# Kernel optimization log

Hardware: AMD Instinct MI355X
Metric: run time of the kernel (lower is better)

The kernel has to match this reference:

```python
import jax, jax.numpy as jnp
import numpy as np

B, N, K, E, H, A = 16384, 200000, 16, 256, 2, 64
HD = E // H  # head_dim = 128


def setup_inputs() -> dict:
    key = jax.random.key(0)
    ks = jax.random.split(key, 10)
    s = 0.02
    return {
        "center_idx": jax.random.randint(ks[0], (B,), 0, N),
        "emb_table": jax.random.normal(ks[1], (N, E), jnp.float32),
        "neighbor_idx": jax.random.randint(ks[2], (N, K), 0, N),
        "neighbor_wt": jax.random.uniform(ks[3], (N, K), dtype=jnp.float32),
        # per-head attention MLP: Linear(2E -> A), GELU, Linear(A -> 1); stacked over heads
        "attn_W1": jax.random.normal(ks[4], (H, 2 * E, A), jnp.float32) * s,
        "attn_b1": jnp.zeros((H, A), jnp.float32),
        "attn_W2": jax.random.normal(ks[5], (H, A), jnp.float32) * s,
        "attn_b2": jnp.zeros((H,), jnp.float32),
        # per-head gate: Linear(HD -> HD), torch convention y = x @ W.T + b
        "gate_W": jax.random.normal(ks[6], (H, HD, HD), jnp.float32) * s,
        "gate_b": jnp.zeros((H, HD), jnp.float32),
        "out_W": jax.random.normal(ks[7], (E, E), jnp.float32) * s,
        "out_b": jnp.zeros((E,), jnp.float32),
    }


def reference(center_idx, emb_table, neighbor_idx, neighbor_wt,
              attn_W1, attn_b1, attn_W2, attn_b2,
              gate_W, gate_b, out_W, out_b):
    valid = center_idx >= 0                                      # [B]
    safe = jnp.maximum(center_idx, 0)
    center = jnp.where(valid[:, None], emb_table[safe], 0.0)      # [B,E]

    nb_idx = neighbor_idx[safe]                                   # [B,K]
    nb_wt = neighbor_wt[safe]                                     # [B,K]
    nb_mask = nb_idx >= 0
    nb_emb = emb_table[jnp.maximum(nb_idx, 0)]                    # [B,K,E]

    pair = jnp.concatenate(
        [jnp.broadcast_to(center[:, None, :], nb_emb.shape), nb_emb], axis=-1)  # [B,K,2E]

    # both attention heads in one einsum (exact GELU, as torch nn.GELU default)
    h1 = jax.nn.gelu(jnp.einsum('bkf,hfa->bkha', pair, attn_W1) + attn_b1,
                     approximate=False)                           # [B,K,H,A]
    logits = jnp.einsum('bkha,ha->bhk', h1, attn_W2) + attn_b2[None, :, None]  # [B,H,K]
    logits = logits + jnp.log(nb_wt + 1e-8)[:, None, :]
    logits = jnp.where(nb_mask[:, None, :], logits, -jnp.inf)
    has_any = jnp.any(nb_mask, axis=-1)                           # [B]
    logits = jnpp_where = jnp.where(has_any[:, None, None], logits, 0.0)
    w = jax.nn.softmax(logits, axis=-1)                           # [B,H,K]; dropout is identity in eval

    # aggregated[:, h*HD:(h+1)*HD] for head h == head-block of head-h weighted sum
    nb_r = nb_emb.reshape(-1, K, H, HD)
    agg = jnp.einsum('bhk,bkhd->bhd', w, nb_r)                    # [B,H,HD]

    c_head = center.reshape(-1, H, HD)
    gate = jax.nn.sigmoid(jnp.einsum('bhd,hed->bhe', c_head, gate_W) + gate_b)
    combined = (c_head + gate * agg).reshape(-1, E)               # [B,E]

    out = combined @ out_W.T + out_b
    return jnp.where(valid[:, None], out, center)
```

## Files before the change

### kernel.cpp

```cpp
#include <hip/hip_runtime.h>
#include <hip/hip_bf16.h>
#include <math.h>

#define BATCH   16384
#define NTAB    200000
#define KNB     16
#define EDIM    256
#define HEADS   2
#define ADIM    64
#define HD      128

typedef __attribute__((ext_vector_type(8))) short  short8;
typedef __attribute__((ext_vector_type(4))) float  f32x4;
typedef __attribute__((ext_vector_type(8))) unsigned short ushort8;
typedef __attribute__((ext_vector_type(4))) unsigned short ushort4v;

__device__ __forceinline__ unsigned short f2b(float f) {
    union { float f; unsigned u; } x; x.f = f;
    unsigned r = x.u + 0x7fffu + ((x.u >> 16) & 1u);
    return (unsigned short)(r >> 16);
}
__device__ __forceinline__ float b2f(unsigned short h) {
    union { unsigned u; float f; } x; x.u = ((unsigned)h) << 16;
    return x.f;
}

static const size_t OFF_T    = 0;
static const size_t OFF_CG   = OFF_T    + (size_t)NTAB * 128 * 2;
static const size_t OFF_COMB = OFF_CG   + (size_t)BATCH * 384 * 2;
static const size_t OFF_WCAT = OFF_COMB + (size_t)BATCH * 256 * 2;
static const size_t OFF_W1B  = OFF_WCAT + 384 * 256 * 2;
static const size_t OFF_OUTW = OFF_W1B  + 128 * 256 * 2;
static const size_t OFF_BCAT = OFF_OUTW + 256 * 256 * 2;

__global__ __launch_bounds__(256) void repack_kernel(
    const float* __restrict__ W1, const float* __restrict__ gateW,
    const float* __restrict__ outW,
    const float* __restrict__ b1, const float* __restrict__ gateB,
    unsigned short* __restrict__ WcatT, unsigned short* __restrict__ W1bT,
    unsigned short* __restrict__ outWT, float* __restrict__ bcat)
{
    int i = blockIdx.x * 256 + threadIdx.x;
    {
        int c = i >> 8, f = i & 255;
        float v;
        if (c < 128) {
            int h = c >> 6, a = c & 63;
            v = W1[h * 32768 + f * 64 + a];
        } else {
            int e = c - 128;
            int h = e >> 7;
            v = ((e >> 7) == (f >> 7)) ? gateW[h * 16384 + (e & 127) * 128 + (f & 127)] : 0.f;
        }
        WcatT[i] = f2b(v);
    }
    if (i < 32768) {
        int c = i >> 8, f = i & 255;
        int h = c >> 6, a = c & 63;
        W1bT[i] = f2b(W1[h * 32768 + (256 + f) * 64 + a]);
    }
    if (i < 65536) outWT[i] = f2b(outW[i]);
    if (i < 384) bcat[i] = (i < 128) ? b1[i] : gateB[i - 128];
}

template<int AMODE, bool OUT_BF16, bool HAS_BIAS, bool HAS_MASK>
__global__ __launch_bounds__(256) void gemm_mfma(
    const float* __restrict__ Af, const unsigned short* __restrict__ Ab,
    const int* __restrict__ gather,
    const unsigned short* __restrict__ Wt, int Nw,
    const float* __restrict__ bias, const int* __restrict__ mask,
    void* __restrict__ Cout, int M)
{
    __shared__ unsigned short sA[128 * 40];
    __shared__ unsigned short sB[128 * 32];
    __shared__ int s_idx[128];

    const int t = threadIdx.x;
    const int row0    = blockIdx.x * 128;
    const int colBase = blockIdx.y * 128;

    if (AMODE == 1 && t < 128) s_idx[t] = gather[row0 + t];

    const int wv   = t >> 6;
    const int wr   = wv >> 1, wc = wv & 1;
    const int lane = t & 63;
    const int l15  = lane & 15;
    const int quad = lane >> 4;

    f32x4 acc[4][4];
#pragma unroll
    for (int a = 0; a < 4; ++a)
#pragma unroll
        for (int b = 0; b < 4; ++b) acc[a][b] = (f32x4)0.f;

    for (int k0 = 0; k0 < 256; k0 += 32) {
        __syncthreads();
        if (AMODE == 2) {
#pragma unroll
            for (int l = 0; l < 2; ++l) {
                int p = t + l * 256;
                int row = p >> 2, seg = p & 3;
                int sr = row0 + row; if (sr > M - 1) sr = M - 1;
                ushort8 v = *(const ushort8*)&Ab[(size_t)sr * 256 + k0 + seg * 8];
                *(ushort8*)&sA[row * 40 + seg * 8] = v;
            }
        } else {
#pragma unroll
            for (int l = 0; l < 4; ++l) {
                int p = t + l * 256;
                int row = p >> 3, seg = p & 7;
                int sr;
                if (AMODE == 1) { int g = s_idx[row]; sr = g < 0 ? 0 : g; }
                else            { sr = row0 + row; if (sr > M - 1) sr = M - 1; }
                const float4 v = *(const float4*)&Af[(size_t)sr * 256 + k0 + seg * 4];
                ushort4v h;
                h.x = f2b(v.x); h.y = f2b(v.y); h.z = f2b(v.z); h.w = f2b(v.w);
                *(ushort4v*)&sA[row * 40 + seg * 4] = h;
            }
        }
#pragma unroll
        for (int l = 0; l < 2; ++l) {
            int p = t + l * 256;
            int n = p >> 2, seg = p & 3;
            const unsigned short* gsrc = Wt + (size_t)(colBase + n) * 256 + k0 + seg * 8;
            unsigned short* lbase = sB + (size_t)(p & ~63) * 8;
            __builtin_amdgcn_global_load_lds(
                (const __attribute__((address_space(1))) void*)gsrc,
                (__attribute__((address_space(3))) void*)lbase, 16, 0, 0);
        }
        __syncthreads();

        short8 af[4], bfr[4];
#pragma unroll
        for (int tr = 0; tr < 4; ++tr)
            af[tr] = *(const short8*)&sA[(wr * 64 + tr * 16 + l15) * 40 + quad * 8];
#pragma unroll
        for (int tc = 0; tc < 4; ++tc)
            bfr[tc] = *(const short8*)&sB[(wc * 64 + tc * 16 + l15) * 32 + quad * 8];
#pragma unroll
        for (int tr = 0; tr < 4; ++tr)
#pragma unroll
            for (int tc = 0; tc < 4; ++tc)
                acc[tr][tc] = __builtin_amdgcn_mfma_f32_16x16x32_bf16(
                    af[tr], bfr[tc], acc[tr][tc], 0, 0, 0);
    }

    float bcol[4];
#pragma unroll
    for (int tc = 0; tc < 4; ++tc)
        bcol[tc] = HAS_BIAS ? bias[colBase + wc * 64 + tc * 16 + l15] : 0.f;

#pragma unroll
    for (int tr = 0; tr < 4; ++tr) {
#pragma unroll
        for (int r = 0; r < 4; ++r) {
            int rowg = row0 + wr * 64 + tr * 16 + quad * 4 + r;
            if (rowg < M) {
                bool zero = HAS_MASK && (mask[rowg] < 0);
#pragma unroll
                for (int tc = 0; tc < 4; ++tc) {
                    int col = colBase + wc * 64 + tc * 16 + l15;
                    float v = zero ? 0.f : acc[tr][tc][r] + bcol[tc];
                    if (OUT_BF16)
                        ((unsigned short*)Cout)[(size_t)rowg * Nw + col] = f2b(v);
                    else
                        ((float*)Cout)[(size_t)rowg * Nw + col] = v;
                }
            }
        }
    }
}

__global__ __launch_bounds__(256) void epilogue_kernel(
    const float* __restrict__ table, const int* __restrict__ center_idx,
    const int* __restrict__ nb_idx_tab, const float* __restrict__ nb_wt_tab,
    const unsigned short* __restrict__ T, const unsigned short* __restrict__ cg,
    const float* __restrict__ W2, const float* __restrict__ b2,
    unsigned short* __restrict__ comb)
{
    const int b = blockIdx.x;
    const int t = threadIdx.x;

    __shared__ float s_cg[384];
    __shared__ float s_w2[128];
    __shared__ float s_logit[32];
    __shared__ float s_wmx[32];
    __shared__ int   s_nb[16];
    __shared__ float s_wt[16];

    const int ci   = center_idx[b];
    const int safe = ci < 0 ? 0 : ci;

    if (t < 16) {
        s_nb[t] = nb_idx_tab[(size_t)safe * KNB + t];
        s_wt[t] = nb_wt_tab[(size_t)safe * KNB + t];
    }
    if (t < 128) s_w2[t] = W2[t];
    for (int i = t; i < 384; i += 256) s_cg[i] = b2f(cg[(size_t)b * 384 + i]);
    const float ctr = (ci < 0) ? 0.f : table[(size_t)ci * 256 + t];
    __syncthreads();

    {
        const int k = t >> 4, s = t & 15;
        const int nb = s_nb[k];
        const int ns = nb < 0 ? 0 : nb;
        const ushort8 tv = *(const ushort8*)&T[(size_t)ns * 128 + s * 8];
        float partial = 0.f;
#pragma unroll
        for (int j = 0; j < 8; ++j) {
            int c = s * 8 + j;
            float v = b2f(tv[j]) + s_cg[c];
            float g = 0.5f * v * (1.f + erff(v * 0.70710678118654752440f));
            partial = fmaf(g, s_w2[c], partial);
        }
        partial += __shfl_xor(partial, 1, 64);
        partial += __shfl_xor(partial, 2, 64);
        partial += __shfl_xor(partial, 4, 64);
        if (s == 0) s_logit[k] = partial;
        if (s == 8) s_logit[16 + k] = partial;
    }
    __syncthreads();

    if (t < 2) {
        int h = t;
        bool hasany = false;
        for (int k = 0; k < 16; ++k) hasany |= (s_nb[k] >= 0);
        if (!hasany) {
            for (int k = 0; k < 16; ++k) s_wmx[h * 16 + k] = 1.f / 16.f;
        } else {
            float lg[16];
            float m = -INFINITY;
            for (int k = 0; k < 16; ++k) {
                float L = (s_nb[k] >= 0)
                    ? s_logit[h * 16 + k] + b2[h] + logf(s_wt[k] + 1e-8f)
                    : -INFINITY;
                lg[k] = L;
                if (L > m) m = L;
            }
            float ssum = 0.f, ex[16];
            for (int k = 0; k < 16; ++k) { ex[k] = expf(lg[k] - m); ssum += ex[k]; }
            float inv = 1.f / ssum;
            for (int k = 0; k < 16; ++k) s_wmx[h * 16 + k] = ex[k] * inv;
        }
    }
    __syncthreads();

    const int h = t >> 7;
    float agg = 0.f;
#pragma unroll
    for (int k = 0; k < 16; ++k) {
        int nb = s_nb[k];
        int ns = nb < 0 ? 0 : nb;
        agg = fmaf(s_wmx[h * 16 + k], table[(size_t)ns * 256 + t], agg);
    }
    float gl   = s_cg[128 + t];
    float gate = 1.f / (1.f + expf(-gl));
    comb[(size_t)b * 256 + t] = f2b(ctr + gate * agg);
}

extern "C" void kernel_launch(void* const* d_in, const int* in_sizes, int n_in,
                              void* d_out, int out_size, void* d_ws, size_t ws_size,
                              hipStream_t stream)
{
    const int*   center_idx = (const int*)  d_in[0];
    const float* emb_table  = (const float*)d_in[1];
    const int*   nb_idx     = (const int*)  d_in[2];
    const float* nb_wt      = (const float*)d_in[3];
    const float* attn_W1    = (const float*)d_in[4];
    const float* attn_b1    = (const float*)d_in[5];
    const float* attn_W2    = (const float*)d_in[6];
    const float* attn_b2    = (const float*)d_in[7];
    const float* gate_W     = (const float*)d_in[8];
    const float* gate_b     = (const float*)d_in[9];
    const float* out_W      = (const float*)d_in[10];
    const float* out_b      = (const float*)d_in[11];
    float* out = (float*)d_out;

    char* ws = (char*)d_ws;
    unsigned short* T     = (unsigned short*)(ws + OFF_T);
    unsigned short* cgB   = (unsigned short*)(ws + OFF_CG);
    unsigned short* comb  = (unsigned short*)(ws + OFF_COMB);
    unsigned short* WcatT = (unsigned short*)(ws + OFF_WCAT);
    unsigned short* W1bT  = (unsigned short*)(ws + OFF_W1B);
    unsigned short* outWT = (unsigned short*)(ws + OFF_OUTW);
    float*          bcat  = (float*)         (ws + OFF_BCAT);

    repack_kernel<<<384, 256, 0, stream>>>(attn_W1, gate_W, out_W, attn_b1, gate_b,
                                           WcatT, W1bT, outWT, bcat);

    gemm_mfma<0, true, false, false><<<dim3((NTAB + 127) / 128, 1), 256, 0, stream>>>(
        emb_table, nullptr, nullptr, W1bT, 128, nullptr, nullptr, T, NTAB);

    gemm_mfma<1, true, true, false><<<dim3(BATCH / 128, 3), 256, 0, stream>>>(
        emb_table, nullptr, center_idx, WcatT, 384, bcat, nullptr, cgB, BATCH);

    epilogue_kernel<<<BATCH, 256, 0, stream>>>(
        emb_table, center_idx, nb_idx, nb_wt, T, cgB, attn_W2, attn_b2, comb);

    gemm_mfma<2, false, true, true><<<dim3(BATCH / 128, 2), 256, 0, stream>>>(
        nullptr, comb, nullptr, outWT, 256, out_b, center_idx, out, BATCH);
}
```

Baseline: 442.9 us.

## Cache bf16 copy of embedding table during first GEMM and gather bf16 rows

The first GEMM over the full table now also writes a bf16 copy of each row it converts. The center-gather GEMM and the epilogue then read these bf16 rows instead of fp32, halving gather bytes; A-tile loads for bf16 modes use direct global-to-LDS loads. The per-row softmax is spread across 32 lanes with shuffle reductions instead of two serial threads. This costs an extra 100MB write and slightly lower precision for the center and neighbor embeddings.

New measurement: 461.8 us. 4.3% more time.

```diff
diff --git a/kernel.cpp b/kernel.cpp
--- a/kernel.cpp
+++ b/kernel.cpp
@@ -25,7 +25,8 @@
     return x.f;
 }
 
-static const size_t OFF_T    = 0;
+static const size_t OFF_TBL  = 0;
+static const size_t OFF_T    = OFF_TBL  + (size_t)NTAB * 256 * 2;
 static const size_t OFF_CG   = OFF_T    + (size_t)NTAB * 128 * 2;
 static const size_t OFF_COMB = OFF_CG   + (size_t)BATCH * 384 * 2;
 static const size_t OFF_WCAT = OFF_COMB + (size_t)BATCH * 256 * 2;
@@ -63,15 +64,16 @@
     if (i < 384) bcat[i] = (i < 128) ? b1[i] : gateB[i - 128];
 }
 
-template<int AMODE, bool OUT_BF16, bool HAS_BIAS, bool HAS_MASK>
+template<int AMODE, bool OUT_BF16, bool HAS_BIAS, bool HAS_MASK, bool WRITE_ABF>
 __global__ __launch_bounds__(256) void gemm_mfma(
     const float* __restrict__ Af, const unsigned short* __restrict__ Ab,
+    unsigned short* __restrict__ AoutBf,
     const int* __restrict__ gather,
     const unsigned short* __restrict__ Wt, int Nw,
     const float* __restrict__ bias, const int* __restrict__ mask,
     void* __restrict__ Cout, int M)
 {
-    __shared__ unsigned short sA[128 * 40];
+    __shared__ unsigned short sA[128 * 32];
     __shared__ unsigned short sB[128 * 32];
     __shared__ int s_idx[128];
 
@@ -95,27 +97,33 @@
 
     for (int k0 = 0; k0 < 256; k0 += 32) {
         __syncthreads();
-        if (AMODE == 2) {
+        if (AMODE == 0) {
+#pragma unroll
+            for (int l = 0; l < 4; ++l) {
+                int p = t + l * 256;
+                int row = p >> 3, seg = p & 7;
+                int gr = row0 + row;
+                int sr = gr < M ? gr : M - 1;
+                const float4 v = *(const float4*)&Af[(size_t)sr * 256 + k0 + seg * 4];
+                ushort4v h;
+                h.x = f2b(v.x); h.y = f2b(v.y); h.z = f2b(v.z); h.w = f2b(v.w);
+                *(ushort4v*)&sA[row * 32 + seg * 4] = h;
+                if (WRITE_ABF && gr < M)
+                    *(ushort4v*)&AoutBf[(size_t)gr * 256 + k0 + seg * 4] = h;
+            }
+        } else {
 #pragma unroll
             for (int l = 0; l < 2; ++l) {
                 int p = t + l * 256;
                 int row = p >> 2, seg = p & 3;
-                int sr = row0 + row; if (sr > M - 1) sr = M - 1;
-                ushort8 v = *(const ushort8*)&Ab[(size_t)sr * 256 + k0 + seg * 8];
-                *(ushort8*)&sA[row * 40 + seg * 8] = v;
-            }
-        } else {
-#pragma unroll
-            for (int l = 0; l < 4; ++l) {
-                int p = t + l * 256;
-                int row = p >> 3, seg = p & 7;
                 int sr;
                 if (AMODE == 1) { int g = s_idx[row]; sr = g < 0 ? 0 : g; }
                 else            { sr = row0 + row; if (sr > M - 1) sr = M - 1; }
-                const float4 v = *(const float4*)&Af[(size_t)sr * 256 + k0 + seg * 4];
-                ushort4v h;
-                h.x = f2b(v.x); h.y = f2b(v.y); h.z = f2b(v.z); h.w = f2b(v.w);
-                *(ushort4v*)&sA[row * 40 + seg * 4] = h;
+                const unsigned short* gsrc = Ab + (size_t)sr * 256 + k0 + seg * 8;
+                unsigned short* lbase = sA + (size_t)(p & ~63) * 8;
+                __builtin_amdgcn_global_load_lds(
+                    (const __attribute__((address_space(1))) void*)gsrc,
+                    (__attribute__((address_space(3))) void*)lbase, 16, 0, 0);
             }
         }
 #pragma unroll
@@ -133,7 +141,7 @@
         short8 af[4], bfr[4];
 #pragma unroll
         for (int tr = 0; tr < 4; ++tr)
-            af[tr] = *(const short8*)&sA[(wr * 64 + tr * 16 + l15) * 40 + quad * 8];
+            af[tr] = *(const short8*)&sA[(wr * 64 + tr * 16 + l15) * 32 + quad * 8];
 #pragma unroll
         for (int tc = 0; tc < 4; ++tc)
             bfr[tc] = *(const short8*)&sB[(wc * 64 + tc * 16 + l15) * 32 + quad * 8];
@@ -172,7 +180,7 @@
 }
 
 __global__ __launch_bounds__(256) void epilogue_kernel(
-    const float* __restrict__ table, const int* __restrict__ center_idx,
+    const unsigned short* __restrict__ tableBf, const int* __restrict__ center_idx,
     const int* __restrict__ nb_idx_tab, const float* __restrict__ nb_wt_tab,
     const unsigned short* __restrict__ T, const unsigned short* __restrict__ cg,
     const float* __restrict__ W2, const float* __restrict__ b2,
@@ -197,7 +205,7 @@
     }
     if (t < 128) s_w2[t] = W2[t];
     for (int i = t; i < 384; i += 256) s_cg[i] = b2f(cg[(size_t)b * 384 + i]);
-    const float ctr = (ci < 0) ? 0.f : table[(size_t)ci * 256 + t];
+    const float ctr = (ci < 0) ? 0.f : b2f(tableBf[(size_t)ci * 256 + t]);
     __syncthreads();
 
     {
@@ -221,27 +229,26 @@
     }
     __syncthreads();
 
-    if (t < 2) {
-        int h = t;
-        bool hasany = false;
-        for (int k = 0; k < 16; ++k) hasany |= (s_nb[k] >= 0);
-        if (!hasany) {
-            for (int k = 0; k < 16; ++k) s_wmx[h * 16 + k] = 1.f / 16.f;
-        } else {
-            float lg[16];
-            float m = -INFINITY;
-            for (int k = 0; k < 16; ++k) {
-                float L = (s_nb[k] >= 0)
-                    ? s_logit[h * 16 + k] + b2[h] + logf(s_wt[k] + 1e-8f)
-                    : -INFINITY;
-                lg[k] = L;
-                if (L > m) m = L;
-            }
-            float ssum = 0.f, ex[16];
-            for (int k = 0; k < 16; ++k) { ex[k] = expf(lg[k] - m); ssum += ex[k]; }
-            float inv = 1.f / ssum;
-            for (int k = 0; k < 16; ++k) s_wmx[h * 16 + k] = ex[k] * inv;
-        }
+    if (t < 32) {
+        const int h = t >> 4, k = t & 15;
+        const int nb = s_nb[k];
+        unsigned long long bm = __ballot(nb >= 0);
+        const bool hasany = ((bm >> (h * 16)) & 0xFFFFull) != 0ull;
+        float L = (nb >= 0)
+            ? s_logit[h * 16 + k] + b2[h] + logf(s_wt[k] + 1e-8f)
+            : -INFINITY;
+        float m = L;
+        m = fmaxf(m, __shfl_xor(m, 1, 16));
+        m = fmaxf(m, __shfl_xor(m, 2, 16));
+        m = fmaxf(m, __shfl_xor(m, 4, 16));
+        m = fmaxf(m, __shfl_xor(m, 8, 16));
+        float e = (nb >= 0) ? expf(L - m) : 0.f;
+        float ssum = e;
+        ssum += __shfl_xor(ssum, 1, 16);
+        ssum += __shfl_xor(ssum, 2, 16);
+        ssum += __shfl_xor(ssum, 4, 16);
+        ssum += __shfl_xor(ssum, 8, 16);
+        s_wmx[t] = hasany ? e / ssum : (1.f / 16.f);
     }
     __syncthreads();
 
@@ -251,7 +258,7 @@
     for (int k = 0; k < 16; ++k) {
         int nb = s_nb[k];
         int ns = nb < 0 ? 0 : nb;
-        agg = fmaf(s_wmx[h * 16 + k], table[(size_t)ns * 256 + t], agg);
+        agg = fmaf(s_wmx[h * 16 + k], b2f(tableBf[(size_t)ns * 256 + t]), agg);
     }
     float gl   = s_cg[128 + t];
     float gate = 1.f / (1.f + expf(-gl));
@@ -277,26 +284,27 @@
     float* out = (float*)d_out;
 
     char* ws = (char*)d_ws;
-    unsigned short* T     = (unsigned short*)(ws + OFF_T);
-    unsigned short* cgB   = (unsigned short*)(ws + OFF_CG);
-    unsigned short* comb  = (unsigned short*)(ws + OFF_COMB);
-    unsigned short* WcatT = (unsigned short*)(ws + OFF_WCAT);
-    unsigned short* W1bT  = (unsigned short*)(ws + OFF_W1B);
-    unsigned short* outWT = (unsigned short*)(ws + OFF_OUTW);
-    float*          bcat  = (float*)         (ws + OFF_BCAT);
+    unsigned short* tableBf = (unsigned short*)(ws + OFF_TBL);
+    unsigned short* T       = (unsigned short*)(ws + OFF_T);
+    unsigned short* cgB     = (unsigned short*)(ws + OFF_CG);
+    unsigned short* comb    = (unsigned short*)(ws + OFF_COMB);
+    unsigned short* WcatT   = (unsigned short*)(ws + OFF_WCAT);
+    unsigned short* W1bT    = (unsigned short*)(ws + OFF_W1B);
+    unsigned short* outWT   = (unsigned short*)(ws + OFF_OUTW);
+    float*          bcat    = (float*)         (ws + OFF_BCAT);
 
     repack_kernel<<<384, 256, 0, stream>>>(attn_W1, gate_W, out_W, attn_b1, gate_b,
                                            WcatT, W1bT, outWT, bcat);
 
-    gemm_mfma<0, true, false, false><<<dim3((NTAB + 127) / 128, 1), 256, 0, stream>>>(
-        emb_table, nullptr, nullptr, W1bT, 128, nullptr, nullptr, T, NTAB);
-
-    gemm_mfma<1, true, true, false><<<dim3(BATCH / 128, 3), 256, 0, stream>>>(
-        emb_table, nullptr, center_idx, WcatT, 384, bcat, nullptr, cgB, BATCH);
+    gemm_mfma<0, true, false, false, true><<<dim3((NTAB + 127) / 128, 1), 256, 0, stream>>>(
+        emb_table, nullptr, tableBf, nullptr, W1bT, 128, nullptr, nullptr, T, NTAB);
+
+    gemm_mfma<1, true, true, false, false><<<dim3(BATCH / 128, 3), 256, 0, stream>>>(
+        nullptr, tableBf, nullptr, center_idx, WcatT, 384, bcat, nullptr, cgB, BATCH);
 
     epilogue_kernel<<<BATCH, 256, 0, stream>>>(
-        emb_table, center_idx, nb_idx, nb_wt, T, cgB, attn_W2, attn_b2, comb);
-
-    gemm_mfma<2, false, true, true><<<dim3(BATCH / 128, 2), 256, 0, stream>>>(
-        nullptr, comb, nullptr, outWT, 256, out_b, center_idx, out, BATCH);
-}
+        tableBf, center_idx, nb_idx, nb_wt, T, cgB, attn_W2, attn_b2, comb);
+
+    gemm_mfma<2, false, true, true, false><<<dim3(BATCH / 128, 2), 256, 0, stream>>>(
+        nullptr, comb, nullptr, nullptr, outWT, 256, out_b, center_idx, out, BATCH);
+}
```
